# Kernel tuning notes

Measured on AMD Instinct MI355X. Metric: run time of the kernel, lower is better.

Reference implementation:

```python
import jax, jax.numpy as jnp
import numpy as np

N = 20000      # num nodes
E = 320000     # num edges
H = 128        # hidden_size
NGATES = 16
NSAGE = 3      # layers 0,1,2 are SAGEConv; layer 3 is GATConv
NEDGE = 2      # edge MLP layers


def setup_inputs() -> dict:
    key = jax.random.key(0)
    ks = jax.random.split(key, 20)
    Hh = H // 2
    s = 0.05
    inp = {
        "shapes": jax.random.randint(ks[0], (N, 1), 1, 5).astype(jnp.float32),
        "gate_ids": jax.random.randint(ks[1], (N,), 0, NGATES),
        "edge_index": jax.random.randint(ks[2], (2, E), 0, N),
        "emb_table": jax.random.normal(ks[3], (NGATES, Hh), jnp.float32) * s,
        "dimW": jax.random.normal(ks[4], (1, Hh), jnp.float32) * s,
        "dimb": jnp.zeros((Hh,), jnp.float32),
        "sage_Wl": jax.random.normal(ks[5], (NSAGE, H, H), jnp.float32) * s,
        "sage_bl": jnp.zeros((NSAGE, H), jnp.float32),
        "sage_Wr": jax.random.normal(ks[6], (NSAGE, H, H), jnp.float32) * s,
        "gat_W": jax.random.normal(ks[7], (H, H), jnp.float32) * s,
        "gat_asrc": jax.random.normal(ks[8], (H,), jnp.float32) * s,
        "gat_adst": jax.random.normal(ks[9], (H,), jnp.float32) * s,
        "gat_b": jnp.zeros((H,), jnp.float32),
        "edgeW": jax.random.normal(ks[10], (NEDGE, H, H), jnp.float32) * s,
        "edgeb": jnp.zeros((NEDGE, H), jnp.float32),
        "outW": jax.random.normal(ks[11], (H, 1), jnp.float32) * s,
        "outb": jnp.zeros((1,), jnp.float32),
    }
    return inp


def _mean_aggr(x, src, dst, n):
    # mean over incoming messages x[src] per destination node
    ssum = jax.ops.segment_sum(x[src], dst, num_segments=n)
    cnt = jax.ops.segment_sum(jnp.ones((src.shape[0],), x.dtype), dst, num_segments=n)
    return ssum / jnp.maximum(cnt, 1.0)[:, None]


def _sage(x, src, dst, Wl, bl, Wr, n):
    # SAGEConv: lin_l(mean_j x_j) + lin_r(x_i)
    return _mean_aggr(x, src, dst, n) @ Wl + bl + x @ Wr


def _gat(x, src, dst, W, a_src, a_dst, b, n):
    # GATConv (1 head, add_self_loops=True)
    loops = jnp.arange(n)
    s = jnp.concatenate([src, loops])
    d = jnp.concatenate([dst, loops])
    h = x @ W
    e = jax.nn.leaky_relu(h[s] @ a_src + h[d] @ a_dst, negative_slope=0.2)
    m = jax.ops.segment_max(e, d, num_segments=n)
    p = jnp.exp(e - m[d])
    z = jax.ops.segment_sum(p, d, num_segments=n)
    alpha = p / z[d]
    return jax.ops.segment_sum(alpha[:, None] * h[s], d, num_segments=n) + b


def reference(shapes, gate_ids, edge_index, emb_table, dimW, dimb, sage_Wl, sage_bl,
              sage_Wr, gat_W, gat_asrc, gat_adst, gat_b, edgeW, edgeb, outW, outb):
    src, dst = edge_index[0], edge_index[1]
    # node features: [dim_layer(shape_rank) ; mean-embedding-bag(gates)]
    x = jnp.concatenate([shapes @ dimW + dimb, emb_table[gate_ids]], axis=1)  # [N,H]
    for i in range(4):
        if i % 4 == 3:
            x = _gat(x, src, dst, gat_W, gat_asrc, gat_adst, gat_b, N)
        else:
            x = _sage(x, src, dst, sage_Wl[i], sage_bl[i], sage_Wr[i], N)
        x = jax.nn.relu(x)
    e = x[src] + x[dst]  # [E,H] edge features
    for j in range(NEDGE):
        e = jax.nn.relu(e @ edgeW[j] + edgeb[j])
    scores = e @ outW + outb  # [E,1]; argmin(scores) selects edge to contract
    return scores
```

## Files before the change

kernel.cpp:

```cpp
#include <hip/hip_runtime.h>

#define NN 20000
#define NE 320000
#define H  128
#define HH 64

typedef short bf16x8 __attribute__((ext_vector_type(8)));
typedef float f32x4  __attribute__((ext_vector_type(4)));

__device__ __forceinline__ float lrelu(float v){ return fmaxf(v, 0.2f*v); }
__device__ __forceinline__ float as_f(unsigned u){ return __uint_as_float(u); }

__device__ __forceinline__ unsigned pk_bf16(float a, float b){
  unsigned r;
  asm("v_cvt_pk_bf16_f32 %0, %1, %2" : "=v"(r) : "v"(a), "v"(b));
  return r;
}

__global__ __launch_bounds__(256) void k_node_init(
    const float* __restrict__ shapes, const int* __restrict__ gid,
    const float* __restrict__ emb, const float* __restrict__ dimW,
    const float* __restrict__ dimb, float* __restrict__ x)
{
  int idx = blockIdx.x*256 + threadIdx.x;
  if (idx >= NN*H) return;
  int n = idx >> 7, j = idx & 127;
  float v;
  if (j < HH) v = shapes[n]*dimW[j] + dimb[j];
  else        v = emb[gid[n]*HH + (j-HH)];
  x[idx] = v;
}

__global__ __launch_bounds__(256) void k_count(const int* __restrict__ dst, int* __restrict__ deg){
  int e = blockIdx.x*256 + threadIdx.x;
  if (e < NE) atomicAdd(&deg[dst[e]], 1);
}

__global__ __launch_bounds__(1024) void k_scan(const int* __restrict__ deg, int* __restrict__ off){
  __shared__ int ps[1024];
  int t = threadIdx.x;
  const int CH = (NN + 1023)/1024;
  int base = t*CH;
  int s = 0;
  for (int i=0;i<CH;i++){ int g=base+i; if (g<NN) s += deg[g]; }
  ps[t] = s; __syncthreads();
  for (int d=1; d<1024; d<<=1){
    int v = (t>=d) ? ps[t-d] : 0;
    __syncthreads();
    ps[t] += v;
    __syncthreads();
  }
  int run = (t==0) ? 0 : ps[t-1];
  for (int i=0;i<CH;i++){ int g=base+i; if (g<NN){ off[g]=run; run += deg[g]; } }
  if (t==1023) off[NN] = run;
}

__global__ __launch_bounds__(256) void k_fill(const int* __restrict__ src, const int* __restrict__ dst,
    const int* __restrict__ off, int* __restrict__ cur, int* __restrict__ csr){
  int e = blockIdx.x*256 + threadIdx.x;
  if (e < NE){
    int d = dst[e];
    int p = atomicAdd(&cur[d], 1);
    csr[off[d]+p] = src[e];
  }
}

__global__ __launch_bounds__(256) void k_aggr(const float* __restrict__ x,
    const int* __restrict__ off, const int* __restrict__ csr, float* __restrict__ agg)
{
  int wid = (blockIdx.x*256 + threadIdx.x) >> 6;
  int lane = threadIdx.x & 63;
  if (wid >= NN) return;
  int b = off[wid], e = off[wid+1];
  float ax=0.f, ay=0.f;
  for (int i=b;i<e;i++){
    int s = csr[i];
    float2 v = *(const float2*)&x[(size_t)s*H + lane*2];
    ax += v.x; ay += v.y;
  }
  float inv = 1.0f / fmaxf((float)(e-b), 1.0f);
  *(float2*)&agg[(size_t)wid*H + lane*2] = make_float2(ax*inv, ay*inv);
}

__global__ __launch_bounds__(256) void k_gat(
    const float* __restrict__ h, const float* __restrict__ hs, const float* __restrict__ hd,
    const int* __restrict__ off, const int* __restrict__ csr,
    const float* __restrict__ bias, float* __restrict__ y)
{
  int wid = (blockIdx.x*256 + threadIdx.x) >> 6;
  int lane = threadIdx.x & 63;
  if (wid >= NN) return;
  int b = off[wid], e = off[wid+1];
  float hdv = hd[wid];
  float eself = lrelu(hs[wid] + hdv);
  float m = eself;
  for (int i=b;i<e;i++) m = fmaxf(m, lrelu(hs[csr[i]] + hdv));
  float z = expf(eself - m);
  float2 hv = *(const float2*)&h[(size_t)wid*H + lane*2];
  float ax = z*hv.x, ay = z*hv.y;
  for (int i=b;i<e;i++){
    int s = csr[i];
    float p = expf(lrelu(hs[s] + hdv) - m);
    z += p;
    float2 u = *(const float2*)&h[(size_t)s*H + lane*2];
    ax = fmaf(p, u.x, ax);
    ay = fmaf(p, u.y, ay);
  }
  float inv = 1.0f / z;
  float2 bv = *(const float2*)&bias[lane*2];
  *(float2*)&y[(size_t)wid*H + lane*2] =
      make_float2(fmaxf(ax*inv + bv.x, 0.f), fmaxf(ay*inv + bv.y, 0.f));
}


__global__ __launch_bounds__(256) void k_wconv_multi(
    const float* __restrict__ edgeW, const float* __restrict__ Wl,
    const float* __restrict__ Wr, const float* __restrict__ gatW,
    uint4* __restrict__ outw)
{
  int t = blockIdx.x*256 + threadIdx.x;
  int m = t >> 11;
  int r = t & 2047;
  int hf = r >> 10, bw = (r >> 6) & 15, s = r & 63;
  const float* W;
  if      (m < 2) W = edgeW + (size_t)m*16384;
  else if (m < 5) W = Wl    + (size_t)(m-2)*16384;
  else if (m < 8) W = Wr    + (size_t)(m-5)*16384;
  else            W = gatW;
  int row0 = (bw & 3)*32 + (s >> 4)*8;
  int col  = hf*64 + (bw >> 2)*16 + (s & 15);
  const float* p = W + row0*128 + col;
  float f[8];
  #pragma unroll
  for (int j=0;j<8;j++) f[j] = p[j*128];
  unsigned h0=pk_bf16(f[0],f[1]), h1=pk_bf16(f[2],f[3]),
           h2=pk_bf16(f[4],f[5]), h3=pk_bf16(f[6],f[7]);
  unsigned l0=pk_bf16(f[0]-as_f(h0<<16), f[1]-as_f(h0&0xffff0000u));
  unsigned l1=pk_bf16(f[2]-as_f(h1<<16), f[3]-as_f(h1&0xffff0000u));
  unsigned l2=pk_bf16(f[4]-as_f(h2<<16), f[5]-as_f(h2&0xffff0000u));
  unsigned l3=pk_bf16(f[6]-as_f(h3<<16), f[7]-as_f(h3&0xffff0000u));
  int base = m*4096 + hf*2048;
  outw[base + bw*64 + s]        = make_uint4(h0,h1,h2,h3);
  outw[base + 1024 + bw*64 + s] = make_uint4(l0,l1,l2,l3);
}

__device__ __forceinline__ void copyW(const uint4* __restrict__ srcw, uint4* R, int tid){
  #pragma unroll
  for (int i=0;i<8;i++) R[tid + i*256] = srcw[tid + i*256];
}

template<int HF>
__device__ __forceinline__ void mfma_half(f32x4* acc, const bf16x8* ah, const bf16x8* al,
                                          const uint4* R, int l)
{
  #pragma unroll
  for (int ntl=0; ntl<4; ntl++){
    f32x4 a = acc[HF*4 + ntl];
    #pragma unroll
    for (int kc=0; kc<4; kc++){
      bf16x8 bh = __builtin_bit_cast(bf16x8, R[(ntl*4+kc)*64 + l]);
      bf16x8 bl = __builtin_bit_cast(bf16x8, R[1024 + (ntl*4+kc)*64 + l]);
      a = __builtin_amdgcn_mfma_f32_16x16x32_bf16(ah[kc], bh, a, 0, 0, 0);
      a = __builtin_amdgcn_mfma_f32_16x16x32_bf16(ah[kc], bl, a, 0, 0, 0);
      a = __builtin_amdgcn_mfma_f32_16x16x32_bf16(al[kc], bh, a, 0, 0, 0);
    }
    acc[HF*4 + ntl] = a;
  }
}

__device__ __forceinline__ void stageA(const float* __restrict__ Ap, bool valid, int g8,
                                       bf16x8* ah, bf16x8* al)
{
  #pragma unroll
  for (int kc=0;kc<4;kc++){
    float f[8];
    if (valid){
      float4 u = *(const float4*)&Ap[kc*32 + g8];
      float4 v = *(const float4*)&Ap[kc*32 + g8 + 4];
      f[0]=u.x; f[1]=u.y; f[2]=u.z; f[3]=u.w; f[4]=v.x; f[5]=v.y; f[6]=v.z; f[7]=v.w;
    } else {
      #pragma unroll
      for (int j=0;j<8;j++) f[j]=0.f;
    }
    unsigned hp[4], lp[4];
    #pragma unroll
    for (int q=0;q<4;q++){
      unsigned hh = pk_bf16(f[2*q], f[2*q+1]);
      hp[q] = hh;
      lp[q] = pk_bf16(f[2*q]-as_f(hh<<16), f[2*q+1]-as_f(hh & 0xffff0000u));
    }
    ah[kc] = __builtin_bit_cast(bf16x8, make_uint4(hp[0],hp[1],hp[2],hp[3]));
    al[kc] = __builtin_bit_cast(bf16x8, make_uint4(lp[0],lp[1],lp[2],lp[3]));
  }
}

template<bool TWO, bool GATEP>
__global__ __launch_bounds__(256) void k_ngemm(
    const float* __restrict__ A1, const float* __restrict__ A2,
    const uint4* __restrict__ wc1, const uint4* __restrict__ wc2,
    const float* __restrict__ bias, float* __restrict__ Y,
    const float* __restrict__ asrc, const float* __restrict__ adst,
    float* __restrict__ hs, float* __restrict__ hd, int M)
{
  __shared__ uint4 R[2048];
  const int tid = threadIdx.x;
  const int l = tid & 63, w = tid >> 6;
  const int row0 = blockIdx.x*64;
  const int arow = row0 + w*16 + (l&15);
  const bool avld = arow < M;
  const int g8 = (l>>4)*8;

  bf16x8 ah[4], al[4];
  stageA(A1 + (size_t)arow*H, avld, g8, ah, al);

  f32x4 acc[8];
  #pragma unroll
  for (int i=0;i<8;i++) acc[i] = 0.f;

  copyW(wc1, R, tid); __syncthreads();
  mfma_half<0>(acc, ah, al, R, l);
  __syncthreads(); copyW(wc1 + 2048, R, tid); __syncthreads();
  mfma_half<1>(acc, ah, al, R, l);

  if constexpr (TWO){
    stageA(A2 + (size_t)arow*H, avld, g8, ah, al);
    __syncthreads(); copyW(wc2, R, tid); __syncthreads();
    mfma_half<0>(acc, ah, al, R, l);
    __syncthreads(); copyW(wc2 + 2048, R, tid); __syncthreads();
    mfma_half<1>(acc, ah, al, R, l);
  }

  if constexpr (!GATEP){
    float bv[8];
    #pragma unroll
    for (int nt=0;nt<8;nt++) bv[nt] = bias[nt*16 + (l&15)];
    #pragma unroll
    for (int r=0;r<4;r++){
      int srow = row0 + w*16 + (l>>4)*4 + r;
      if (srow < M){
        #pragma unroll
        for (int nt=0;nt<8;nt++)
          Y[(size_t)srow*H + nt*16 + (l&15)] = fmaxf(acc[nt][r] + bv[nt], 0.f);
      }
    }
  } else {
    float avv[8], dvv[8];
    #pragma unroll
    for (int nt=0;nt<8;nt++){
      avv[nt] = asrc[nt*16 + (l&15)];
      dvv[nt] = adst[nt*16 + (l&15)];
    }
    #pragma unroll
    for (int r=0;r<4;r++){
      int srow = row0 + w*16 + (l>>4)*4 + r;
      float sp = 0.f, dp = 0.f;
      #pragma unroll
      for (int nt=0;nt<8;nt++){
        float hv = acc[nt][r];
        sp = fmaf(hv, avv[nt], sp);
        dp = fmaf(hv, dvv[nt], dp);
        if (srow < M) Y[(size_t)srow*H + nt*16 + (l&15)] = hv;
      }
      #pragma unroll
      for (int mm=1; mm<16; mm<<=1){
        sp += __shfl_xor(sp, mm, 16);
        dp += __shfl_xor(dp, mm, 16);
      }
      if ((l&15)==0 && srow < M){ hs[srow] = sp; hd[srow] = dp; }
    }
  }
}

__global__ __launch_bounds__(256) void k_edge_mfma(
    const float* __restrict__ x, const int* __restrict__ src, const int* __restrict__ dst,
    const uint4* __restrict__ wcvt,
    const float* __restrict__ b1, const float* __restrict__ b2,
    const float* __restrict__ outW, const float* __restrict__ outb,
    float* __restrict__ out)
{
  __shared__ uint4 R[2048];
  const int tid = threadIdx.x;
  const int l = tid & 63, w = tid >> 6;
  const int e0 = blockIdx.x * 64;

  {
    int e = e0 + l;
    int sn = src[e], dn = dst[e];
    const float4* ps = (const float4*)(x + (size_t)sn*H + w*32);
    const float4* pd = (const float4*)(x + (size_t)dn*H + w*32);
    float ev[32];
    #pragma unroll
    for (int q=0;q<8;q++){
      float4 a = ps[q], b = pd[q];
      ev[q*4+0]=a.x+b.x; ev[q*4+1]=a.y+b.y; ev[q*4+2]=a.z+b.z; ev[q*4+3]=a.w+b.w;
    }
    int blk = ((l>>4)*4 + w)*64;
    #pragma unroll
    for (int g=0; g<4; g++){
      unsigned hp[4], lp[4];
      #pragma unroll
      for (int q=0;q<4;q++){
        float f0 = ev[g*8+q*2], f1 = ev[g*8+q*2+1];
        unsigned h = pk_bf16(f0, f1);
        hp[q] = h;
        lp[q] = pk_bf16(f0 - as_f(h<<16), f1 - as_f(h & 0xffff0000u));
      }
      int ai = blk + (l&15) + 16*g;
      R[ai]        = make_uint4(hp[0],hp[1],hp[2],hp[3]);
      R[1024 + ai] = make_uint4(lp[0],lp[1],lp[2],lp[3]);
    }
  }
  __syncthreads();

  bf16x8 ah[4], al[4];
  #pragma unroll
  for (int kc=0; kc<4; kc++){
    ah[kc] = __builtin_bit_cast(bf16x8, R[(w*4+kc)*64 + l]);
    al[kc] = __builtin_bit_cast(bf16x8, R[1024 + (w*4+kc)*64 + l]);
  }
  __syncthreads();
  copyW(wcvt + 0*2048, R, tid);
  __syncthreads();

  f32x4 acc[8];
  #pragma unroll
  for (int i=0;i<8;i++) acc[i] = 0.f;
  mfma_half<0>(acc, ah, al, R, l);
  __syncthreads();
  copyW(wcvt + 1*2048, R, tid);
  __syncthreads();
  mfma_half<1>(acc, ah, al, R, l);
  __syncthreads();

  {
    float b1v[8];
    #pragma unroll
    for (int nt=0;nt<8;nt++) b1v[nt] = b1[nt*16 + (l&15)];
    #pragma unroll
    for (int nt=0;nt<8;nt++){
      int b2blk = w*4 + (nt>>1);
      int gp = (2*nt + ((l&15)>>3)) & 3;
      #pragma unroll
      for (int r=0;r<4;r++){
        float v = fmaxf(acc[nt][r] + b1v[nt], 0.f);
        unsigned h = pk_bf16(v, v);
        unsigned lo = pk_bf16(v - as_f(h<<16), 0.f);
        int sp = (4*(l>>4) + r) + 16*gp;
        int off = (b2blk*64 + sp)*16 + (l&7)*2;
        *(short*)((char*)R + off)         = (short)(h  & 0xffff);
        *(short*)((char*)R + 16384 + off) = (short)(lo & 0xffff);
      }
    }
  }
  #pragma unroll
  for (int kc=0; kc<4; kc++){
    ah[kc] = __builtin_bit_cast(bf16x8, R[(w*4+kc)*64 + l]);
    al[kc] = __builtin_bit_cast(bf16x8, R[1024 + (w*4+kc)*64 + l]);
  }
  __syncthreads();
  copyW(wcvt + 2*2048, R, tid);
  __syncthreads();

  f32x4 acc2[8];
  #pragma unroll
  for (int i=0;i<8;i++) acc2[i] = 0.f;
  mfma_half<0>(acc2, ah, al, R, l);
  __syncthreads();
  copyW(wcvt + 3*2048, R, tid);
  __syncthreads();
  mfma_half<1>(acc2, ah, al, R, l);

  {
    float b2v[8], owv[8];
    #pragma unroll
    for (int nt=0;nt<8;nt++){
      b2v[nt] = b2[nt*16 + (l&15)];
      owv[nt] = outW[nt*16 + (l&15)];
    }
    float ob = outb[0];
    #pragma unroll
    for (int r=0;r<4;r++){
      float p = 0.f;
      #pragma unroll
      for (int nt=0;nt<8;nt++)
        p = fmaf(fmaxf(acc2[nt][r] + b2v[nt], 0.f), owv[nt], p);
      #pragma unroll
      for (int m=1;m<16;m<<=1) p += __shfl_xor(p, m, 16);
      if ((l&15)==0) out[e0 + w*16 + (l>>4)*4 + r] = p + ob;
    }
  }
}

extern "C" void kernel_launch(void* const* d_in, const int* in_sizes, int n_in,
                              void* d_out, int out_size, void* d_ws, size_t ws_size,
                              hipStream_t stream)
{
  const float* shapes   = (const float*)d_in[0];
  const int*   gate_ids = (const int*)  d_in[1];
  const int*   ei       = (const int*)  d_in[2];
  const float* emb      = (const float*)d_in[3];
  const float* dimW     = (const float*)d_in[4];
  const float* dimb     = (const float*)d_in[5];
  const float* sage_Wl  = (const float*)d_in[6];
  const float* sage_bl  = (const float*)d_in[7];
  const float* sage_Wr  = (const float*)d_in[8];
  const float* gat_W    = (const float*)d_in[9];
  const float* gat_asrc = (const float*)d_in[10];
  const float* gat_adst = (const float*)d_in[11];
  const float* gat_b    = (const float*)d_in[12];
  const float* edgeW    = (const float*)d_in[13];
  const float* edgeb    = (const float*)d_in[14];
  const float* outW     = (const float*)d_in[15];
  const float* outb     = (const float*)d_in[16];
  const int* src = ei;
  const int* dst = ei + NE;

  char* w = (char*)d_ws;
  auto alloc = [&](size_t bytes)->void* {
    void* p = (void*)w; w += (bytes + 255) & ~(size_t)255; return p;
  };
  float* xa   = (float*)alloc((size_t)NN*H*4);
  float* xb   = (float*)alloc((size_t)NN*H*4);
  float* agg  = (float*)alloc((size_t)NN*H*4);
  float* hs   = (float*)alloc((size_t)NN*4);
  float* hd   = (float*)alloc((size_t)NN*4);
  int*   deg  = (int*)alloc((size_t)NN*4);
  int*   off  = (int*)alloc((size_t)(NN+1)*4);
  int*   cur  = (int*)alloc((size_t)NN*4);
  int*   csr  = (int*)alloc((size_t)NE*4);
  uint4* wcvt = (uint4*)alloc((size_t)9*4096*16);

  hipMemsetAsync(deg, 0, (size_t)NN*4, stream);
  hipMemsetAsync(cur, 0, (size_t)NN*4, stream);

  k_node_init<<<(NN*H+255)/256, 256, 0, stream>>>(shapes, gate_ids, emb, dimW, dimb, xa);
  k_count<<<(NE+255)/256, 256, 0, stream>>>(dst, deg);
  k_scan<<<1, 1024, 0, stream>>>(deg, off);
  k_fill<<<(NE+255)/256, 256, 0, stream>>>(src, dst, off, cur, csr);
  k_wconv_multi<<<72, 256, 0, stream>>>(edgeW, sage_Wl, sage_Wr, gat_W, wcvt);

  float* xin = xa; float* xout = xb;
  const int gemm_blocks = (NN+63)/64;
  for (int i=0;i<3;i++){
    k_aggr<<<NN/4, 256, 0, stream>>>(xin, off, csr, agg);
    k_ngemm<true,false><<<gemm_blocks, 256, 0, stream>>>(
        agg, xin, wcvt + (size_t)(2+i)*4096, wcvt + (size_t)(5+i)*4096,
        sage_bl + (size_t)i*H, xout, nullptr, nullptr, nullptr, nullptr, NN);
    float* t = xin; xin = xout; xout = t;
  }

  k_ngemm<false,true><<<gemm_blocks, 256, 0, stream>>>(
      xin, nullptr, wcvt + (size_t)8*4096, nullptr,
      nullptr, agg, gat_asrc, gat_adst, hs, hd, NN);
  k_gat<<<NN/4, 256, 0, stream>>>(agg, hs, hd, off, csr, gat_b, xout);
  { float* t = xin; xin = xout; xout = t; }

  k_edge_mfma<<<NE/64, 256, 0, stream>>>(xin, src, dst, wcvt,
      edgeb, edgeb + H, outW, outb, (float*)d_out);
}
```

Measured before the change: 472.8 us.

## Process edges in destination-sorted order with XCD swizzle; unroll gather loops

```diff
diff --git a/kernel.cpp b/kernel.cpp
--- a/kernel.cpp
+++ b/kernel.cpp
@@ -56,12 +56,16 @@
 }
 
 __global__ __launch_bounds__(256) void k_fill(const int* __restrict__ src, const int* __restrict__ dst,
-    const int* __restrict__ off, int* __restrict__ cur, int* __restrict__ csr){
+    const int* __restrict__ off, int* __restrict__ cur, int* __restrict__ csr,
+    int* __restrict__ dstA, int* __restrict__ eidA){
   int e = blockIdx.x*256 + threadIdx.x;
   if (e < NE){
     int d = dst[e];
     int p = atomicAdd(&cur[d], 1);
-    csr[off[d]+p] = src[e];
+    int pos = off[d] + p;
+    csr[pos]  = src[e];
+    dstA[pos] = d;
+    eidA[pos] = e;
   }
 }
 
@@ -72,12 +76,24 @@
   int lane = threadIdx.x & 63;
   if (wid >= NN) return;
   int b = off[wid], e = off[wid+1];
-  float ax=0.f, ay=0.f;
-  for (int i=b;i<e;i++){
+  float ax0=0.f, ay0=0.f, ax1=0.f, ay1=0.f, ax2=0.f, ay2=0.f, ax3=0.f, ay3=0.f;
+  int i = b;
+  for (; i+3 < e; i += 4){
+    int s0=csr[i], s1=csr[i+1], s2=csr[i+2], s3=csr[i+3];
+    float2 v0 = *(const float2*)&x[(size_t)s0*H + lane*2];
+    float2 v1 = *(const float2*)&x[(size_t)s1*H + lane*2];
+    float2 v2 = *(const float2*)&x[(size_t)s2*H + lane*2];
+    float2 v3 = *(const float2*)&x[(size_t)s3*H + lane*2];
+    ax0+=v0.x; ay0+=v0.y; ax1+=v1.x; ay1+=v1.y;
+    ax2+=v2.x; ay2+=v2.y; ax3+=v3.x; ay3+=v3.y;
+  }
+  for (; i < e; ++i){
     int s = csr[i];
     float2 v = *(const float2*)&x[(size_t)s*H + lane*2];
-    ax += v.x; ay += v.y;
-  }
+    ax0 += v.x; ay0 += v.y;
+  }
+  float ax = (ax0+ax1)+(ax2+ax3);
+  float ay = (ay0+ay1)+(ay2+ay3);
   float inv = 1.0f / fmaxf((float)(e-b), 1.0f);
   *(float2*)&agg[(size_t)wid*H + lane*2] = make_float2(ax*inv, ay*inv);
 }
@@ -94,11 +110,35 @@
   float hdv = hd[wid];
   float eself = lrelu(hs[wid] + hdv);
   float m = eself;
-  for (int i=b;i<e;i++) m = fmaxf(m, lrelu(hs[csr[i]] + hdv));
+  int i = b;
+  for (; i+3 < e; i += 4){
+    float l0 = lrelu(hs[csr[i]]   + hdv);
+    float l1 = lrelu(hs[csr[i+1]] + hdv);
+    float l2 = lrelu(hs[csr[i+2]] + hdv);
+    float l3 = lrelu(hs[csr[i+3]] + hdv);
+    m = fmaxf(m, fmaxf(fmaxf(l0,l1), fmaxf(l2,l3)));
+  }
+  for (; i < e; ++i) m = fmaxf(m, lrelu(hs[csr[i]] + hdv));
+
   float z = expf(eself - m);
   float2 hv = *(const float2*)&h[(size_t)wid*H + lane*2];
   float ax = z*hv.x, ay = z*hv.y;
-  for (int i=b;i<e;i++){
+  i = b;
+  for (; i+3 < e; i += 4){
+    int s0=csr[i], s1=csr[i+1], s2=csr[i+2], s3=csr[i+3];
+    float p0 = expf(lrelu(hs[s0] + hdv) - m);
+    float p1 = expf(lrelu(hs[s1] + hdv) - m);
+    float p2 = expf(lrelu(hs[s2] + hdv) - m);
+    float p3 = expf(lrelu(hs[s3] + hdv) - m);
+    z += (p0+p1)+(p2+p3);
+    float2 u0 = *(const float2*)&h[(size_t)s0*H + lane*2];
+    float2 u1 = *(const float2*)&h[(size_t)s1*H + lane*2];
+    float2 u2 = *(const float2*)&h[(size_t)s2*H + lane*2];
+    float2 u3 = *(const float2*)&h[(size_t)s3*H + lane*2];
+    ax = fmaf(p0,u0.x, fmaf(p1,u1.x, fmaf(p2,u2.x, fmaf(p3,u3.x, ax))));
+    ay = fmaf(p0,u0.y, fmaf(p1,u1.y, fmaf(p2,u2.y, fmaf(p3,u3.y, ay))));
+  }
+  for (; i < e; ++i){
     int s = csr[i];
     float p = expf(lrelu(hs[s] + hdv) - m);
     z += p;
@@ -272,8 +312,8 @@
 }
 
 __global__ __launch_bounds__(256) void k_edge_mfma(
-    const float* __restrict__ x, const int* __restrict__ src, const int* __restrict__ dst,
-    const uint4* __restrict__ wcvt,
+    const float* __restrict__ x, const int* __restrict__ csr, const int* __restrict__ dstA,
+    const int* __restrict__ eidA, const uint4* __restrict__ wcvt,
     const float* __restrict__ b1, const float* __restrict__ b2,
     const float* __restrict__ outW, const float* __restrict__ outb,
     float* __restrict__ out)
@@ -281,11 +321,14 @@
   __shared__ uint4 R[2048];
   const int tid = threadIdx.x;
   const int l = tid & 63, w = tid >> 6;
-  const int e0 = blockIdx.x * 64;
-
+  const int bid = blockIdx.x;
+  const int e0 = ((bid & 7)*625 + (bid >> 3)) * 64;
+
+  int eid;
   {
-    int e = e0 + l;
-    int sn = src[e], dn = dst[e];
+    int i = e0 + l;
+    int sn = csr[i], dn = dstA[i];
+    eid = eidA[i];
     const float4* ps = (const float4*)(x + (size_t)sn*H + w*32);
     const float4* pd = (const float4*)(x + (size_t)dn*H + w*32);
     float ev[32];
@@ -386,7 +429,9 @@
         p = fmaf(fmaxf(acc2[nt][r] + b2v[nt], 0.f), owv[nt], p);
       #pragma unroll
       for (int m=1;m<16;m<<=1) p += __shfl_xor(p, m, 16);
-      if ((l&15)==0) out[e0 + w*16 + (l>>4)*4 + r] = p + ob;
+      int row = w*16 + (l>>4)*4 + r;
+      int eo = __shfl(eid, row);
+      if ((l&15)==0) out[eo] = p + ob;
     }
   }
 }
@@ -428,6 +473,8 @@
   int*   off  = (int*)alloc((size_t)(NN+1)*4);
   int*   cur  = (int*)alloc((size_t)NN*4);
   int*   csr  = (int*)alloc((size_t)NE*4);
+  int*   dstA = (int*)alloc((size_t)NE*4);
+  int*   eidA = (int*)alloc((size_t)NE*4);
   uint4* wcvt = (uint4*)alloc((size_t)9*4096*16);
 
   hipMemsetAsync(deg, 0, (size_t)NN*4, stream);
@@ -436,7 +483,7 @@
   k_node_init<<<(NN*H+255)/256, 256, 0, stream>>>(shapes, gate_ids, emb, dimW, dimb, xa);
   k_count<<<(NE+255)/256, 256, 0, stream>>>(dst, deg);
   k_scan<<<1, 1024, 0, stream>>>(deg, off);
-  k_fill<<<(NE+255)/256, 256, 0, stream>>>(src, dst, off, cur, csr);
+  k_fill<<<(NE+255)/256, 256, 0, stream>>>(src, dst, off, cur, csr, dstA, eidA);
   k_wconv_multi<<<72, 256, 0, stream>>>(edgeW, sage_Wl, sage_Wr, gat_W, wcvt);
 
   float* xin = xa; float* xout = xb;
@@ -455,6 +502,6 @@
   k_gat<<<NN/4, 256, 0, stream>>>(agg, hs, hd, off, csr, gat_b, xout);
   { float* t = xin; xin = xout; xout = t; }
 
-  k_edge_mfma<<<NE/64, 256, 0, stream>>>(xin, src, dst, wcvt,
+  k_edge_mfma<<<NE/64, 256, 0, stream>>>(xout==xa?xb:xa, csr, dstA, eidA, wcvt,
       edgeb, edgeb + H, outW, outb, (float*)d_out);
 }
```

Result: faster. 400.9 us (-15.2%).
